# Kernel tuning notes

Measured on AMD Instinct MI355X. Metric: run time of the kernel, lower is better.

## Reference

```python
import jax, jax.numpy as jnp
import numpy as np

B, S, D, H = 2, 2048, 1024, 16
DK = D // H  # 64


def _quantum(x, W1, b1, W2, b2):
    # Stand-in for QuantumNeuralLayer: classical->quantum->classical, d_k -> d_k.
    return jnp.tanh(x @ W1 + b1) @ W2 + b2


def setup_inputs() -> dict:
    key = jax.random.key(0)
    ks = jax.random.split(key, 16)
    s = 1.0 / np.sqrt(DK)
    inp = {
        "q": jax.random.normal(ks[0], (B, S, D), dtype=jnp.float32),
        "k": jax.random.normal(ks[1], (B, S, D), dtype=jnp.float32),
        "v": jax.random.normal(ks[2], (B, S, D), dtype=jnp.float32),
    }
    names = ["q", "k", "v"]
    for i, n in enumerate(names):
        inp[f"W{n}1"] = jax.random.normal(ks[3 + 4 * i], (DK, DK), dtype=jnp.float32) * s
        inp[f"b{n}1"] = jnp.zeros((DK,), dtype=jnp.float32)
        inp[f"W{n}2"] = jax.random.normal(ks[4 + 4 * i], (DK, DK), dtype=jnp.float32) * s
        inp[f"b{n}2"] = jnp.zeros((DK,), dtype=jnp.float32)
    inp["Wo"] = jax.random.normal(ks[15], (D, D), dtype=jnp.float32) * (1.0 / np.sqrt(D))
    inp["bo"] = jnp.zeros((D,), dtype=jnp.float32)
    return inp


def reference(q, k, v, Wq1, bq1, Wq2, bq2, Wk1, bk1, Wk2, bk2,
              Wv1, bv1, Wv2, bv2, Wo, bo):
    b, s, _ = q.shape
    # split heads: [B, S, H, DK]
    qh = q.reshape(b, s, H, DK)
    kh = k.reshape(b, s, H, DK)
    vh = v.reshape(b, s, H, DK)
    # quantum per-feature transform on last dim
    qh = _quantum(qh, Wq1, bq1, Wq2, bq2)
    kh = _quantum(kh, Wk1, bk1, Wk2, bk2)
    vh = _quantum(vh, Wv1, bv1, Wv2, bv2)
    scale = 1.0 / jnp.sqrt(jnp.asarray(DK, dtype=qh.dtype))
    # scores: [B, H, S, S]
    scores = jnp.einsum("bqhd,bkhd->bhqk", qh, kh) * scale
    attn = jax.nn.softmax(scores, axis=-1)
    # context: [B, H, S, DK] -> [B, S, D]
    ctx = jnp.einsum("bhqk,bkhd->bqhd", attn, vh).reshape(b, s, D)
    return ctx @ Wo + bo
```

## Files before the change

### kernel.cpp

```cpp
#include <hip/hip_runtime.h>

#define B_ 2
#define S_ 2048
#define D_ 1024
#define H_ 16
#define DK_ 64

typedef float f32x4 __attribute__((ext_vector_type(4)));
typedef float f32x16 __attribute__((ext_vector_type(16)));
typedef short bf16x8 __attribute__((ext_vector_type(8)));

static __device__ __forceinline__ unsigned short f2bf(float f) {
  unsigned u = __float_as_uint(f);
  unsigned r = (u + 0x7FFFu + ((u >> 16) & 1u)) >> 16;
  return (unsigned short)r;
}

static __device__ __forceinline__ unsigned cvtpk_bf16(float lo, float hi) {
  unsigned r;
  asm("v_cvt_pk_bf16_f32 %0, %1, %2" : "=v"(r) : "v"(lo), "v"(hi));
  return r;
}

static __device__ __forceinline__ void load16_lds(const void* g, void* lds) {
  __builtin_amdgcn_global_load_lds(
      (const __attribute__((address_space(1))) unsigned int*)g,
      (__attribute__((address_space(3))) unsigned int*)lds, 16, 0, 0);
}

static __device__ __forceinline__ bf16x8 make_pa8(const float* p, int hi) {
  unsigned x1 = cvtpk_bf16(p[0], p[1]);
  unsigned x2 = cvtpk_bf16(p[2], p[3]);
  unsigned y1 = cvtpk_bf16(p[4], p[5]);
  unsigned y2 = cvtpk_bf16(p[6], p[7]);
  unsigned sx1 = (unsigned)__shfl_xor((int)x1, 32);
  unsigned sx2 = (unsigned)__shfl_xor((int)x2, 32);
  unsigned sy1 = (unsigned)__shfl_xor((int)y1, 32);
  unsigned sy2 = (unsigned)__shfl_xor((int)y2, 32);
  union {
    unsigned u[4];
    bf16x8 v;
  } pa;
  pa.u[0] = hi ? sy1 : x1;
  pa.u[1] = hi ? sy2 : x2;
  pa.u[2] = hi ? y1 : sx1;
  pa.u[3] = hi ? y2 : sx2;
  return pa.v;
}

static __device__ __forceinline__ float tanh_fast(float x) {
  float xc = fminf(fmaxf(x, -9.0f), 9.0f);
  float e = exp2f(xc * 2.88539008177792681472f);
  return (e - 1.0f) / (e + 1.0f);
}

__global__ __launch_bounds__(256) void quantum_fused(
    const float* __restrict__ xq, const float* __restrict__ xk,
    const float* __restrict__ xv,
    const float* __restrict__ Wq1, const float* __restrict__ bq1,
    const float* __restrict__ Wq2, const float* __restrict__ bq2,
    const float* __restrict__ Wk1, const float* __restrict__ bk1,
    const float* __restrict__ Wk2, const float* __restrict__ bk2,
    const float* __restrict__ Wv1, const float* __restrict__ bv1,
    const float* __restrict__ Wv2, const float* __restrict__ bv2,
    unsigned short* __restrict__ qhb, unsigned short* __restrict__ khb,
    unsigned short* __restrict__ vtb, float qscale) {
  const int tid = threadIdx.x;
  const int w = tid >> 6;
  const int l = tid & 63;
  const int lq = l & 31;
  const int hi = l >> 5;
  const int bh = blockIdx.y;
  const int b = bh >> 4, h = bh & 15;
  const int s0w = blockIdx.x * 128 + w * 32;

  const float* x;
  const float* W1;
  const float* b1;
  const float* W2;
  const float* b2;
  unsigned short* outp;
  float scale = 1.0f;
  int vmode = 0;
  if (blockIdx.z == 0) {
    x = xq; W1 = Wq1; b1 = bq1; W2 = Wq2; b2 = bq2; outp = qhb;
    scale = qscale;
  } else if (blockIdx.z == 1) {
    x = xk; W1 = Wk1; b1 = bk1; W2 = Wk2; b2 = bk2; outp = khb;
  } else {
    x = xv; W1 = Wv1; b1 = bv1; W2 = Wv2; b2 = bv2; outp = vtb;
    vmode = 1;
  }

  bf16x8 w1f[2][4];
#pragma unroll
  for (int ca = 0; ca < 2; ++ca)
#pragma unroll
    for (int kc = 0; kc < 4; ++kc) {
      const float* wp = W1 + (size_t)(kc * 16 + hi * 8) * 64 + ca * 32 + lq;
      union {
        unsigned u[4];
        bf16x8 v;
      } ww;
#pragma unroll
      for (int jj = 0; jj < 4; ++jj)
        ww.u[jj] = cvtpk_bf16(wp[(2 * jj) * 64], wp[(2 * jj + 1) * 64]);
      w1f[ca][kc] = ww.v;
    }

  const float* xrow = x + (((size_t)b * S_ + s0w + lq) * H_ + h) * DK_;
  bf16x8 xf[4];
#pragma unroll
  for (int kc = 0; kc < 4; ++kc) {
    float4 f0 = *(const float4*)(xrow + kc * 16 + hi * 8);
    float4 f1 = *(const float4*)(xrow + kc * 16 + hi * 8 + 4);
    union {
      unsigned u[4];
      bf16x8 v;
    } xx;
    xx.u[0] = cvtpk_bf16(f0.x, f0.y);
    xx.u[1] = cvtpk_bf16(f0.z, f0.w);
    xx.u[2] = cvtpk_bf16(f1.x, f1.y);
    xx.u[3] = cvtpk_bf16(f1.z, f1.w);
    xf[kc] = xx.v;
  }

  f32x16 acc1[2];
#pragma unroll
  for (int ca = 0; ca < 2; ++ca)
#pragma unroll
    for (int r = 0; r < 16; ++r)
      acc1[ca][r] = b1[ca * 32 + (r & 3) + 8 * (r >> 2) + 4 * hi];
#pragma unroll
  for (int kc = 0; kc < 4; ++kc) {
    acc1[0] = __builtin_amdgcn_mfma_f32_32x32x16_bf16(w1f[0][kc], xf[kc], acc1[0], 0, 0, 0);
    acc1[1] = __builtin_amdgcn_mfma_f32_32x32x16_bf16(w1f[1][kc], xf[kc], acc1[1], 0, 0, 0);
  }

  float t0[16], t1[16];
#pragma unroll
  for (int r = 0; r < 16; ++r) {
    t0[r] = tanh_fast(acc1[0][r]);
    t1[r] = tanh_fast(acc1[1][r]);
  }

  bf16x8 af[4];
  af[0] = make_pa8(&t0[0], hi);
  af[1] = make_pa8(&t0[8], hi);
  af[2] = make_pa8(&t1[0], hi);
  af[3] = make_pa8(&t1[8], hi);

  bf16x8 w2f[2][4];
#pragma unroll
  for (int nb = 0; nb < 2; ++nb)
#pragma unroll
    for (int kc = 0; kc < 4; ++kc) {
      const float* wp = W2 + (size_t)(kc * 16 + hi * 8) * 64 + nb * 32 + lq;
      union {
        unsigned u[4];
        bf16x8 v;
      } ww;
#pragma unroll
      for (int jj = 0; jj < 4; ++jj)
        ww.u[jj] = cvtpk_bf16(wp[(2 * jj) * 64], wp[(2 * jj + 1) * 64]);
      w2f[nb][kc] = ww.v;
    }

  f32x16 acc2[2];
#pragma unroll
  for (int nb = 0; nb < 2; ++nb)
#pragma unroll
    for (int r = 0; r < 16; ++r)
      acc2[nb][r] = b2[nb * 32 + (r & 3) + 8 * (r >> 2) + 4 * hi];
#pragma unroll
  for (int kc = 0; kc < 4; ++kc) {
    acc2[0] = __builtin_amdgcn_mfma_f32_32x32x16_bf16(af[kc], w2f[0][kc], acc2[0], 0, 0, 0);
    acc2[1] = __builtin_amdgcn_mfma_f32_32x32x16_bf16(af[kc], w2f[1][kc], acc2[1], 0, 0, 0);
  }

  if (!vmode) {
#pragma unroll
    for (int nb = 0; nb < 2; ++nb)
#pragma unroll
      for (int r = 0; r < 16; ++r) {
        const int s = s0w + (r & 3) + 8 * (r >> 2) + 4 * hi;
        outp[((size_t)bh * S_ + s) * DK_ + nb * 32 + lq] =
            f2bf(acc2[nb][r] * scale);
      }
  } else {
#pragma unroll
    for (int nb = 0; nb < 2; ++nb) {
      float yv[16];
#pragma unroll
      for (int r = 0; r < 16; ++r) yv[r] = acc2[nb][r];
      const size_t rowb = ((size_t)bh * DK_ + nb * 32 + lq) * S_;
      *(bf16x8*)(outp + rowb + s0w + hi * 8) = make_pa8(&yv[0], hi);
      *(bf16x8*)(outp + rowb + s0w + 16 + hi * 8) = make_pa8(&yv[8], hi);
    }
  }
}

__global__ __launch_bounds__(256) void attn_kernel(
    const unsigned short* __restrict__ qhb,
    const unsigned short* __restrict__ khb,
    const unsigned short* __restrict__ vtb,
    unsigned short* __restrict__ ctxb) {
  __shared__ __align__(16) unsigned short ks_u[2][64 * 64];
  __shared__ __align__(16) unsigned short vs_u[2][64 * 64];

  const int tid = threadIdx.x;
  const int w = tid >> 6;
  const int l = tid & 63;
  const int lq = l & 31;
  const int hi = l >> 5;
  const int bh = blockIdx.x;
  const int b = bh >> 4, h = bh & 15;
  const int q0 = blockIdx.y * 128 + w * 32;

  const unsigned short* qp = qhb + ((size_t)bh * S_ + q0 + lq) * DK_ + hi * 8;
  bf16x8 qf[4];
#pragma unroll
  for (int kc = 0; kc < 4; ++kc) qf[kc] = *(const bf16x8*)(qp + kc * 16);

  f32x16 o0 = {}, o1 = {};
  float m_ = -1e30f, l_ = 0.f;

  const unsigned short* kgbase = khb + (size_t)bh * S_ * DK_;
  const unsigned short* vgbase = vtb + (size_t)bh * DK_ * S_;
  const int r0 = w * 16 + (l >> 3);
  const int sl8 = ((l & 7) ^ (l >> 3)) * 8;

#define STAGE(BUF, TT)                                                        \
  {                                                                           \
    const int tb = (TT)*64;                                                   \
    char* kb = (char*)ks_u[BUF] + w * 2048;                                   \
    char* vb = (char*)vs_u[BUF] + w * 2048;                                   \
    load16_lds(kgbase + (size_t)(tb + r0) * DK_ + sl8, kb);                   \
    load16_lds(kgbase + (size_t)(tb + r0 + 8) * DK_ + sl8, kb + 1024);        \
    load16_lds(vgbase + (size_t)r0 * S_ + tb + sl8, vb);                      \
    load16_lds(vgbase + (size_t)(r0 + 8) * S_ + tb + sl8, vb + 1024);         \
  }

  STAGE(0, 0)
  __syncthreads();

  for (int t = 0; t < 32; ++t) {
    const char* ksP = (const char*)ks_u[t & 1];
    const char* vsP = (const char*)vs_u[t & 1];
    if (t < 31) STAGE((t + 1) & 1, t + 1)

    f32x16 s0 = {}, s1 = {};
#pragma unroll
    for (int kc = 0; kc < 4; ++kc) {
      const int slot = kc * 2 + hi;
      bf16x8 k0 = *(const bf16x8*)(ksP + lq * 128 + ((slot ^ (lq & 7)) << 4));
      bf16x8 k1 = *(const bf16x8*)(ksP + (32 + lq) * 128 + ((slot ^ (lq & 7)) << 4));
      s0 = __builtin_amdgcn_mfma_f32_32x32x16_bf16(k0, qf[kc], s0, 0, 0, 0);
      s1 = __builtin_amdgcn_mfma_f32_32x32x16_bf16(k1, qf[kc], s1, 0, 0, 0);
    }

    float pmax = fmaxf(fmaxf(s0[0], s0[1]), fmaxf(s0[2], s0[3]));
#pragma unroll
    for (int i = 4; i < 16; i += 4)
      pmax = fmaxf(pmax, fmaxf(fmaxf(s0[i], s0[i + 1]), fmaxf(s0[i + 2], s0[i + 3])));
#pragma unroll
    for (int i = 0; i < 16; i += 4)
      pmax = fmaxf(pmax, fmaxf(fmaxf(s1[i], s1[i + 1]), fmaxf(s1[i + 2], s1[i + 3])));
    pmax = fmaxf(pmax, __shfl_xor(pmax, 32));

    if (!__all(pmax <= m_ + 8.0f)) {
      const float mnew = fmaxf(m_, pmax);
      const float scl = exp2f(m_ - mnew);
      m_ = mnew;
      l_ *= scl;
#pragma unroll
      for (int r = 0; r < 16; ++r) {
        const float sr = __shfl(scl, ((r & 3) + 8 * (r >> 2)) + 4 * hi);
        o0[r] *= sr;
        o1[r] *= sr;
      }
    }

#pragma unroll
    for (int i = 0; i < 16; ++i) s0[i] = exp2f(s0[i] - m_);
#pragma unroll
    for (int i = 0; i < 16; ++i) s1[i] = exp2f(s1[i] - m_);
    {
      float t0a = 0.f, t1a = 0.f, t2a = 0.f, t3a = 0.f;
#pragma unroll
      for (int i = 0; i < 16; i += 4) {
        t0a += s0[i] + s1[i];
        t1a += s0[i + 1] + s1[i + 1];
        t2a += s0[i + 2] + s1[i + 2];
        t3a += s0[i + 3] + s1[i + 3];
      }
      float ps = (t0a + t1a) + (t2a + t3a);
      ps += __shfl_xor(ps, 32);
      l_ += ps;
    }

    float pv[8];
    union {
      unsigned u[4];
      bf16x8 v;
    } pa;

#define PV_STEP(SARR, CC, CIDX)                                               \
  {                                                                           \
    _Pragma("unroll") for (int j = 0; j < 8; ++j) pv[j] = SARR[(CC)*8 + j];   \
    pa.v = make_pa8(pv, hi);                                                  \
    const int slot = (CIDX)*2 + hi;                                           \
    bf16x8 v0 = *(const bf16x8*)(vsP + lq * 128 + ((slot ^ (lq & 7)) << 4));  \
    bf16x8 v1 = *(const bf16x8*)(vsP + (32 + lq) * 128 + ((slot ^ (lq & 7)) << 4)); \
    o0 = __builtin_amdgcn_mfma_f32_32x32x16_bf16(pa.v, v0, o0, 0, 0, 0);      \
    o1 = __builtin_amdgcn_mfma_f32_32x32x16_bf16(pa.v, v1, o1, 0, 0, 0);      \
  }

    PV_STEP(s0, 0, 0)
    PV_STEP(s0, 1, 1)
    PV_STEP(s1, 0, 2)
    PV_STEP(s1, 1, 3)
#undef PV_STEP

    __syncthreads();
  }
#undef STAGE

  const float linv = 1.0f / l_;
#pragma unroll
  for (int r = 0; r < 16; ++r) {
    const int crow = ((r & 3) + 8 * (r >> 2)) + 4 * hi;
    const float lr = __shfl(linv, crow);
    const int qg = q0 + crow;
    const size_t base = ((size_t)b * S_ + qg) * D_ + h * DK_;
    ctxb[base + lq] = f2bf(o0[r] * lr);
    ctxb[base + 32 + lq] = f2bf(o1[r] * lr);
  }
}

__global__ __launch_bounds__(256) void wo_transpose(
    const float* __restrict__ Wo, unsigned short* __restrict__ WoT) {
  __shared__ float t[64][65];
  const int k0 = blockIdx.x * 64, n0 = blockIdx.y * 64;
  const int r = threadIdx.x >> 4, c4 = threadIdx.x & 15;
#pragma unroll
  for (int i = 0; i < 4; ++i) {
    float4 v = *(const float4*)&Wo[(size_t)(k0 + r + 16 * i) * D_ + n0 + c4 * 4];
    t[r + 16 * i][c4 * 4 + 0] = v.x;
    t[r + 16 * i][c4 * 4 + 1] = v.y;
    t[r + 16 * i][c4 * 4 + 2] = v.z;
    t[r + 16 * i][c4 * 4 + 3] = v.w;
  }
  __syncthreads();
  const int n = threadIdx.x >> 2, kc = threadIdx.x & 3;
  union {
    unsigned short u[16];
    uint4 v[2];
  } pk;
#pragma unroll
  for (int j = 0; j < 16; ++j) pk.u[j] = f2bf(t[kc * 16 + j][n]);
  unsigned short* op = WoT + (size_t)(n0 + n) * D_ + k0 + kc * 16;
  *(uint4*)op = pk.v[0];
  *(uint4*)(op + 8) = pk.v[1];
}

__global__ __launch_bounds__(256) void out_gemm_mfma(
    const unsigned short* __restrict__ A,
    const unsigned short* __restrict__ BT,
    const float* __restrict__ bo, float* __restrict__ C) {
  __shared__ __align__(16) unsigned short As[128 * 64];
  __shared__ __align__(16) unsigned short Bs[128 * 64];

  const int tid = threadIdx.x;
  const int w = tid >> 6, l = tid & 63;
  const int ll = l & 15, lg = l >> 4;
  const int wr = w >> 1, wc = w & 1;
  const int m0 = blockIdx.y * 128, n0 = blockIdx.x * 128;

  const int srow = l >> 3;
  const int sslot = (l & 7) ^ srow;
  const int g_off = sslot * 8;

  f32x4 acc[4][4];
#pragma unroll
  for (int mt = 0; mt < 4; ++mt)
#pragma unroll
    for (int nt = 0; nt < 4; ++nt) acc[mt][nt] = (f32x4){0.f, 0.f, 0.f, 0.f};

  for (int k0 = 0; k0 < D_; k0 += 64) {
    __syncthreads();
#pragma unroll
    for (int c = 0; c < 4; ++c) {
      const int row = c * 32 + w * 8 + srow;
      load16_lds(A + (size_t)(m0 + row) * D_ + k0 + g_off,
                 (char*)As + c * 4096 + w * 1024);
      load16_lds(BT + (size_t)(n0 + row) * D_ + k0 + g_off,
                 (char*)Bs + c * 4096 + w * 1024);
    }
    __syncthreads();

#pragma unroll
    for (int half = 0; half < 2; ++half) {
      bf16x8 af[4], bfr[4];
#pragma unroll
      for (int mt = 0; mt < 4; ++mt) {
        const int row = wr * 64 + mt * 16 + ll;
        af[mt] = *(const bf16x8*)((const char*)As + row * 128 +
                                  (((half * 4 + lg) ^ (row & 7)) << 4));
      }
#pragma unroll
      for (int nt = 0; nt < 4; ++nt) {
        const int rowb = wc * 64 + nt * 16 + ll;
        bfr[nt] = *(const bf16x8*)((const char*)Bs + rowb * 128 +
                                   (((half * 4 + lg) ^ (rowb & 7)) << 4));
      }
#pragma unroll
      for (int mt = 0; mt < 4; ++mt)
#pragma unroll
        for (int nt = 0; nt < 4; ++nt)
          acc[mt][nt] = __builtin_amdgcn_mfma_f32_16x16x32_bf16(
              af[mt], bfr[nt], acc[mt][nt], 0, 0, 0);
    }
  }

#pragma unroll
  for (int nt = 0; nt < 4; ++nt) {
    const int col = n0 + wc * 64 + nt * 16 + ll;
    const float bv = bo[col];
#pragma unroll
    for (int mt = 0; mt < 4; ++mt) {
      const int row0 = m0 + wr * 64 + mt * 16 + lg * 4;
#pragma unroll
      for (int r = 0; r < 4; ++r)
        C[(size_t)(row0 + r) * D_ + col] = acc[mt][nt][r] + bv;
    }
  }
}

extern "C" void kernel_launch(void* const* d_in, const int* in_sizes, int n_in,
                              void* d_out, int out_size, void* d_ws,
                              size_t ws_size, hipStream_t stream) {
  const float* q = (const float*)d_in[0];
  const float* k = (const float*)d_in[1];
  const float* v = (const float*)d_in[2];
  const float* Wq1 = (const float*)d_in[3];
  const float* bq1 = (const float*)d_in[4];
  const float* Wq2 = (const float*)d_in[5];
  const float* bq2 = (const float*)d_in[6];
  const float* Wk1 = (const float*)d_in[7];
  const float* bk1 = (const float*)d_in[8];
  const float* Wk2 = (const float*)d_in[9];
  const float* bk2 = (const float*)d_in[10];
  const float* Wv1 = (const float*)d_in[11];
  const float* bv1 = (const float*)d_in[12];
  const float* Wv2 = (const float*)d_in[13];
  const float* bv2 = (const float*)d_in[14];
  const float* Wo = (const float*)d_in[15];
  const float* bo = (const float*)d_in[16];
  float* out = (float*)d_out;

  const size_t TEN = (size_t)B_ * H_ * S_ * DK_;
  char* ws = (char*)d_ws;
  unsigned short* qhb = (unsigned short*)ws;
  unsigned short* khb = (unsigned short*)(ws + TEN * 2);
  unsigned short* vtb = (unsigned short*)(ws + TEN * 4);
  unsigned short* ctxb = (unsigned short*)(ws + TEN * 6);
  unsigned short* wot = (unsigned short*)(ws + TEN * 8);

  const float cs = 0.125f * 1.44269504088896340736f;
  quantum_fused<<<dim3(16, 32, 3), 256, 0, stream>>>(
      q, k, v, Wq1, bq1, Wq2, bq2, Wk1, bk1, Wk2, bk2, Wv1, bv1, Wv2, bv2,
      qhb, khb, vtb, cs);
  wo_transpose<<<dim3(16, 16), 256, 0, stream>>>(Wo, wot);

  attn_kernel<<<dim3(32, 16), 256, 0, stream>>>(qhb, khb, vtb, ctxb);

  out_gemm_mfma<<<dim3(8, 32), 256, 0, stream>>>(ctxb, wot, bo, out);
}
```

Before: 122.0 us.

## Triple-buffer LDS with vmcnt-based waits in attention and output GEMM

Both the attention kernel and the output projection GEMM move from double or single buffering to a three-stage LDS ring. Each iteration waits on partial vmcnt counts and a single s_barrier, so loads two tiles ahead stay in flight during compute, and the trailing __syncthreads goes away. MFMA blocks are wrapped in s_setprio to favour the matrix-issuing waves. This uses more LDS per block, which may reduce occupancy, and correctness now depends on hand-counted vmcnt values.

Result: faster. 116.1 us (-4.8%).

```diff
diff --git a/kernel.cpp b/kernel.cpp
--- a/kernel.cpp
+++ b/kernel.cpp
@@ -205,8 +205,8 @@
     const unsigned short* __restrict__ khb,
     const unsigned short* __restrict__ vtb,
     unsigned short* __restrict__ ctxb) {
-  __shared__ __align__(16) unsigned short ks_u[2][64 * 64];
-  __shared__ __align__(16) unsigned short vs_u[2][64 * 64];
+  __shared__ __align__(16) unsigned short ks_u[3][64 * 64];
+  __shared__ __align__(16) unsigned short vs_u[3][64 * 64];
 
   const int tid = threadIdx.x;
   const int w = tid >> 6;
@@ -242,14 +242,25 @@
   }
 
   STAGE(0, 0)
-  __syncthreads();
+  STAGE(1, 1)
 
   for (int t = 0; t < 32; ++t) {
-    const char* ksP = (const char*)ks_u[t & 1];
-    const char* vsP = (const char*)vs_u[t & 1];
-    if (t < 31) STAGE((t + 1) & 1, t + 1)
+    if (t < 31) {
+      asm volatile("s_waitcnt vmcnt(4)" ::: "memory");
+    } else {
+      asm volatile("s_waitcnt vmcnt(0)" ::: "memory");
+    }
+    __builtin_amdgcn_sched_barrier(0);
+    __builtin_amdgcn_s_barrier();
+    __builtin_amdgcn_sched_barrier(0);
+
+    const int cur = t % 3;
+    const char* ksP = (const char*)ks_u[cur];
+    const char* vsP = (const char*)vs_u[cur];
+    if (t < 30) STAGE((t + 2) % 3, t + 2)
 
     f32x16 s0 = {}, s1 = {};
+    __builtin_amdgcn_s_setprio(1);
 #pragma unroll
     for (int kc = 0; kc < 4; ++kc) {
       const int slot = kc * 2 + hi;
@@ -258,6 +269,7 @@
       s0 = __builtin_amdgcn_mfma_f32_32x32x16_bf16(k0, qf[kc], s0, 0, 0, 0);
       s1 = __builtin_amdgcn_mfma_f32_32x32x16_bf16(k1, qf[kc], s1, 0, 0, 0);
     }
+    __builtin_amdgcn_s_setprio(0);
 
     float pmax = fmaxf(fmaxf(s0[0], s0[1]), fmaxf(s0[2], s0[3]));
 #pragma unroll
@@ -316,13 +328,13 @@
     o1 = __builtin_amdgcn_mfma_f32_32x32x16_bf16(pa.v, v1, o1, 0, 0, 0);      \
   }
 
+    __builtin_amdgcn_s_setprio(1);
     PV_STEP(s0, 0, 0)
     PV_STEP(s0, 1, 1)
     PV_STEP(s1, 0, 2)
     PV_STEP(s1, 1, 3)
+    __builtin_amdgcn_s_setprio(0);
 #undef PV_STEP
-
-    __syncthreads();
   }
 #undef STAGE
 
@@ -368,8 +380,8 @@
     const unsigned short* __restrict__ A,
     const unsigned short* __restrict__ BT,
     const float* __restrict__ bo, float* __restrict__ C) {
-  __shared__ __align__(16) unsigned short As[128 * 64];
-  __shared__ __align__(16) unsigned short Bs[128 * 64];
+  __shared__ __align__(16) unsigned short As[3][128 * 64];
+  __shared__ __align__(16) unsigned short Bs[3][128 * 64];
 
   const int tid = threadIdx.x;
   const int w = tid >> 6, l = tid & 63;
@@ -387,17 +399,33 @@
 #pragma unroll
     for (int nt = 0; nt < 4; ++nt) acc[mt][nt] = (f32x4){0.f, 0.f, 0.f, 0.f};
 
-  for (int k0 = 0; k0 < D_; k0 += 64) {
-    __syncthreads();
-#pragma unroll
-    for (int c = 0; c < 4; ++c) {
-      const int row = c * 32 + w * 8 + srow;
-      load16_lds(A + (size_t)(m0 + row) * D_ + k0 + g_off,
-                 (char*)As + c * 4096 + w * 1024);
-      load16_lds(BT + (size_t)(n0 + row) * D_ + k0 + g_off,
-                 (char*)Bs + c * 4096 + w * 1024);
-    }
-    __syncthreads();
+#define STAGE_G(BUF, KT)                                                      \
+  {                                                                           \
+    const int k0e = (KT)*64;                                                  \
+    _Pragma("unroll") for (int c = 0; c < 4; ++c) {                           \
+      const int row = c * 32 + w * 8 + srow;                                  \
+      load16_lds(A + (size_t)(m0 + row) * D_ + k0e + g_off,                   \
+                 (char*)As[BUF] + c * 4096 + w * 1024);                       \
+      load16_lds(BT + (size_t)(n0 + row) * D_ + k0e + g_off,                  \
+                 (char*)Bs[BUF] + c * 4096 + w * 1024);                       \
+    }                                                                         \
+  }
+
+  STAGE_G(0, 0)
+  STAGE_G(1, 1)
+
+  for (int kt = 0; kt < 16; ++kt) {
+    if (kt < 15) {
+      asm volatile("s_waitcnt vmcnt(8)" ::: "memory");
+    } else {
+      asm volatile("s_waitcnt vmcnt(0)" ::: "memory");
+    }
+    __builtin_amdgcn_sched_barrier(0);
+    __builtin_amdgcn_s_barrier();
+    __builtin_amdgcn_sched_barrier(0);
+
+    const int cur = kt % 3;
+    if (kt < 14) STAGE_G((kt + 2) % 3, kt + 2)
 
 #pragma unroll
     for (int half = 0; half < 2; ++half) {
@@ -405,23 +433,26 @@
 #pragma unroll
       for (int mt = 0; mt < 4; ++mt) {
         const int row = wr * 64 + mt * 16 + ll;
-        af[mt] = *(const bf16x8*)((const char*)As + row * 128 +
+        af[mt] = *(const bf16x8*)((const char*)As[cur] + row * 128 +
                                   (((half * 4 + lg) ^ (row & 7)) << 4));
       }
 #pragma unroll
       for (int nt = 0; nt < 4; ++nt) {
         const int rowb = wc * 64 + nt * 16 + ll;
-        bfr[nt] = *(const bf16x8*)((const char*)Bs + rowb * 128 +
+        bfr[nt] = *(const bf16x8*)((const char*)Bs[cur] + rowb * 128 +
                                    (((half * 4 + lg) ^ (rowb & 7)) << 4));
       }
+      __builtin_amdgcn_s_setprio(1);
 #pragma unroll
       for (int mt = 0; mt < 4; ++mt)
 #pragma unroll
         for (int nt = 0; nt < 4; ++nt)
           acc[mt][nt] = __builtin_amdgcn_mfma_f32_16x16x32_bf16(
               af[mt], bfr[nt], acc[mt][nt], 0, 0, 0);
-    }
-  }
+      __builtin_amdgcn_s_setprio(0);
+    }
+  }
+#undef STAGE_G
 
 #pragma unroll
   for (int nt = 0; nt < 4; ++nt) {
```
